# Kernel tuning notes

Measured on AMD Instinct MI355X. Metric: run time of the kernel, lower is better.

## Reference

```python
import jax, jax.numpy as jnp
import numpy as np

T, B = 128, 64
EMB, HID, NTOK = 400, 1152, 33278
# layer dims: (in, out) per layer, matching AWD_LSTM construction
LAYER_DIMS = [(EMB, HID), (HID, HID), (HID, EMB)]


def _uniform(key, shape, bound):
    return jax.random.uniform(key, shape, jnp.float32, -bound, bound)


def setup_inputs() -> dict:
    key = jax.random.key(0)
    ks = jax.random.split(key, 32)
    inp = {
        "x": jax.random.normal(ks[0], (T, B, EMB), jnp.float32),
        "h0_0": jnp.zeros((B, HID), jnp.float32),
        "h0_1": jnp.zeros((B, HID), jnp.float32),
        "h0_2": jnp.zeros((B, EMB), jnp.float32),
        "c0_0": jnp.zeros((B, HID), jnp.float32),
        "c0_1": jnp.zeros((B, HID), jnp.float32),
        "c0_2": jnp.zeros((B, EMB), jnp.float32),
    }
    ki = 1
    for li, (din, dout) in enumerate(LAYER_DIMS):
        bound = 1.0 / np.sqrt(dout)
        inp[f"W_ih{li}"] = _uniform(ks[ki + 0], (4 * dout, din), bound)
        inp[f"W_hh{li}"] = _uniform(ks[ki + 1], (4 * dout, dout), bound)
        inp[f"b_ih{li}"] = _uniform(ks[ki + 2], (4 * dout,), bound)
        inp[f"b_hh{li}"] = _uniform(ks[ki + 3], (4 * dout,), bound)
        ki += 4
    bd = 1.0 / np.sqrt(EMB)
    inp["W_dec"] = _uniform(ks[ki], (NTOK, EMB), bd)
    inp["b_dec"] = _uniform(ks[ki + 1], (NTOK,), bd)
    return inp


def _lstm_cell(x, h, c, W_ih, W_hh, b_ih, b_hh):
    # PyTorch gate order: i, f, g, o
    gates = x @ W_ih.T + b_ih + h @ W_hh.T + b_hh
    i, f, g, o = jnp.split(gates, 4, axis=-1)
    c_new = jax.nn.sigmoid(f) * c + jax.nn.sigmoid(i) * jnp.tanh(g)
    h_new = jax.nn.sigmoid(o) * jnp.tanh(c_new)
    return h_new, c_new


def reference(x, h0_0, h0_1, h0_2, c0_0, c0_1, c0_2,
              W_ih0, W_hh0, b_ih0, b_hh0,
              W_ih1, W_hh1, b_ih1, b_hh1,
              W_ih2, W_hh2, b_ih2, b_hh2,
              W_dec, b_dec):
    params = [(W_ih0, W_hh0, b_ih0, b_hh0),
              (W_ih1, W_hh1, b_ih1, b_hh1),
              (W_ih2, W_hh2, b_ih2, b_hh2)]

    def step(carry, xt):
        hs, cs = carry
        inp = xt
        new_h, new_c = [], []
        for li in range(3):
            h, c = _lstm_cell(inp, hs[li], cs[li], *params[li])
            new_h.append(h)
            new_c.append(c)
            inp = h
        return (tuple(new_h), tuple(new_c)), new_h[-1]

    carry0 = ((h0_0, h0_1, h0_2), (c0_0, c0_1, c0_2))
    (hs, cs), out = jax.lax.scan(step, carry0, x)  # out: (T, B, EMB)
    decoded = out.reshape(T * B, EMB) @ W_dec.T + b_dec
    return decoded.reshape(T, B, NTOK)
```

## Files before the change

kernel.cpp:

```cpp
#include <hip/hip_runtime.h>
#include <math.h>

typedef unsigned short u16;
typedef __attribute__((ext_vector_type(8))) short short8;
typedef __attribute__((ext_vector_type(4))) float f32x4;

__device__ __forceinline__ u16 f32_to_bf16(float x) {
    union { float f; unsigned int u; } v; v.f = x;
    unsigned int u = v.u;
    return (u16)((u + 0x7FFFu + ((u >> 16) & 1u)) >> 16);
}
__device__ __forceinline__ float bf16_to_f32(u16 h) {
    union { unsigned int u; float f; } v; v.u = ((unsigned int)h) << 16; return v.f;
}

__global__ void split_pad_kernel(const float* __restrict__ src,
                                 u16* __restrict__ hi, u16* __restrict__ lo,
                                 int N, int K, int Npad, int Kpad, int perm)
{
    int idx = blockIdx.x * 256 + threadIdx.x;
    if (idx >= Npad * Kpad) return;
    int n = idx / Kpad, k = idx - n * Kpad;
    float x = 0.f;
    if (n < N && k < K) {
        int srow = n;
        if (perm) { int dout = N >> 2; srow = (n & 3) * dout + (n >> 2); }
        x = src[(size_t)srow * K + k];
    }
    u16 h = f32_to_bf16(x);
    hi[idx] = h;
    lo[idx] = f32_to_bf16(x - bf16_to_f32(h));
}

__global__ void bias_perm_kernel(const float* __restrict__ bi,
                                 const float* __restrict__ bh,
                                 float* __restrict__ out, int N4)
{
    int c = blockIdx.x * 256 + threadIdx.x;
    if (c >= N4) return;
    int dout = N4 >> 2;
    int s = (c & 3) * dout + (c >> 2);
    out[c] = bi[s] + bh[s];
}

__global__ __launch_bounds__(256) void gemm3m(
    const float* __restrict__ Af32,
    const u16* __restrict__ Ahi, const u16* __restrict__ Alo,
    const u16* __restrict__ Whi, const u16* __restrict__ Wlo,
    const float* __restrict__ bias,
    float* __restrict__ C,
    int Nreal, int Kreal, int Kp, int lda, int ldc, int amode)
{
    __shared__ __align__(16) u16 As[2][128][32];
    __shared__ __align__(16) u16 Ws[2][128][32];

    const int tid  = threadIdx.x;
    const int lane = tid & 63, wave = tid >> 6;
    const int m0 = blockIdx.y * 128, n0 = blockIdx.x * 128;
    const int wm = (wave >> 1) * 64, wn = (wave & 1) * 64;

    f32x4 acc[4][4];
#pragma unroll
    for (int i = 0; i < 4; ++i)
#pragma unroll
        for (int j = 0; j < 4; ++j)
#pragma unroll
            for (int r = 0; r < 4; ++r) acc[i][j][r] = 0.f;

    const int srow = tid >> 2;
    const int sq   = tid & 3;
    const int dq   = (sq ^ ((srow >> 2) & 3)) * 8;
    const int fr   = lane & 15;
    const int fq   = lane >> 4;
    const int rcol = (fq ^ ((fr >> 2) & 3)) * 8;

    for (int k0 = 0; k0 < Kp; k0 += 32) {
#pragma unroll
        for (int half = 0; half < 2; ++half) {
            int row = half * 64 + srow;
            int kc  = k0 + sq * 8;
            if (amode == 0) {
                union { u16 s[8]; short8 v; } uh, ul;
                if (kc + 8 <= Kreal) {
                    const float* p = &Af32[(size_t)(m0 + row) * lda + kc];
#pragma unroll
                    for (int j = 0; j < 8; ++j) {
                        float xv = p[j];
                        u16 hh = f32_to_bf16(xv);
                        uh.s[j] = hh;
                        ul.s[j] = f32_to_bf16(xv - bf16_to_f32(hh));
                    }
                } else {
#pragma unroll
                    for (int j = 0; j < 8; ++j) { uh.s[j] = 0; ul.s[j] = 0; }
                }
                *(short8*)&As[0][row][dq] = uh.v;
                *(short8*)&As[1][row][dq] = ul.v;
            } else {
                size_t ao = (size_t)(m0 + row) * lda + kc;
                *(short8*)&As[0][row][dq] = *(const short8*)(Ahi + ao);
                *(short8*)&As[1][row][dq] = *(const short8*)(Alo + ao);
            }
            size_t wo = (size_t)(n0 + row) * Kp + kc;
            *(short8*)&Ws[0][row][dq] = *(const short8*)(Whi + wo);
            *(short8*)&Ws[1][row][dq] = *(const short8*)(Wlo + wo);
        }
        __syncthreads();

        short8 ah[4], al[4], wh[4], wl[4];
#pragma unroll
        for (int f = 0; f < 4; ++f) {
            int arow = wm + f * 16 + fr;
            ah[f] = *(const short8*)&As[0][arow][rcol];
            al[f] = *(const short8*)&As[1][arow][rcol];
            int wrow = wn + f * 16 + fr;
            wh[f] = *(const short8*)&Ws[0][wrow][rcol];
            wl[f] = *(const short8*)&Ws[1][wrow][rcol];
        }
#pragma unroll
        for (int i = 0; i < 4; ++i)
#pragma unroll
            for (int j = 0; j < 4; ++j) {
                acc[i][j] = __builtin_amdgcn_mfma_f32_16x16x32_bf16(ah[i], wh[j], acc[i][j], 0, 0, 0);
                acc[i][j] = __builtin_amdgcn_mfma_f32_16x16x32_bf16(ah[i], wl[j], acc[i][j], 0, 0, 0);
                acc[i][j] = __builtin_amdgcn_mfma_f32_16x16x32_bf16(al[i], wh[j], acc[i][j], 0, 0, 0);
            }
        __syncthreads();
    }

#pragma unroll
    for (int j = 0; j < 4; ++j) {
        int n = n0 + wn + j * 16 + fr;
        if (n >= Nreal) continue;
        float bv = bias ? bias[n] : 0.f;
#pragma unroll
        for (int i = 0; i < 4; ++i) {
            int mrow = m0 + wm + i * 16 + fq * 4;
#pragma unroll
            for (int r = 0; r < 4; ++r)
                C[(size_t)(mrow + r) * ldc + n] = acc[i][j][r] + bv;
        }
    }
}

#define PF(S, KT_) do {                                                        \
    int q_ = (((KT_) * 4 + fq) ^ sxor) * 8;                                    \
    a0h_##S = *(const short8*)&Wlds[rA * Kp + q_];                             \
    a0l_##S = *(const short8*)&Wlds[(32 + rA) * Kp + q_];                      \
    a1h_##S = *(const short8*)&Wlds[rB * Kp + q_];                             \
    a1l_##S = *(const short8*)&Wlds[(32 + rB) * Kp + q_];                      \
    hh_##S = *(const short8*)(hrow_hi + (KT_) * 32 + fq * 8);                  \
    hl_##S = *(const short8*)(hrow_lo + (KT_) * 32 + fq * 8);                  \
} while (0)

#define CM(S) do {                                                             \
    accA = __builtin_amdgcn_mfma_f32_16x16x32_bf16(a0h_##S, hh_##S, accA, 0, 0, 0); \
    accB = __builtin_amdgcn_mfma_f32_16x16x32_bf16(a1h_##S, hh_##S, accB, 0, 0, 0); \
    accA = __builtin_amdgcn_mfma_f32_16x16x32_bf16(a0h_##S, hl_##S, accA, 0, 0, 0); \
    accB = __builtin_amdgcn_mfma_f32_16x16x32_bf16(a1h_##S, hl_##S, accB, 0, 0, 0); \
    accA = __builtin_amdgcn_mfma_f32_16x16x32_bf16(a0l_##S, hh_##S, accA, 0, 0, 0); \
    accB = __builtin_amdgcn_mfma_f32_16x16x32_bf16(a1l_##S, hh_##S, accB, 0, 0, 0); \
} while (0)

__global__ __launch_bounds__(256, 1) void persistent_lstm(
    const u16* __restrict__ Whi, const u16* __restrict__ Wlo,
    const u16* __restrict__ h0hi, const u16* __restrict__ h0lo,
    u16* __restrict__ seqHi, u16* __restrict__ seqLo,
    const float* __restrict__ pre,
    const float* __restrict__ c_in, float* __restrict__ c_out,
    int* __restrict__ gcnt,
    int* __restrict__ rootc,
    int* __restrict__ go,
    int t0, int N4, int Kp, int dout, int G)
{
    extern __shared__ __align__(16) u16 Wlds[];
    const int tid  = threadIdx.x;
    const int lane = tid & 63, wave = tid >> 6;
    const int fr = lane & 15, fq = lane >> 4;
    const int c0blk = blockIdx.x * 32;
    const int CH = Kp >> 3;
    const int b = wave * 16 + fr;
    const int grp = blockIdx.x & 7;
    const int gsz = (G - grp + 7) >> 3;

    for (int idx = tid; idx < 64 * CH; idx += 256) {
        int buf = idx / (32 * CH);
        int rem = idx - buf * 32 * CH;
        int r = rem / CH, q = rem - r * CH;
        const u16* src = buf ? Wlo : Whi;
        short8 v = *(const short8*)(src + (size_t)(c0blk + r) * Kp + q * 8);
        *(short8*)&Wlds[(buf * 32 + r) * Kp + (q ^ (r & 7)) * 8] = v;
    }

    const int cA = c0blk + fq * 4;
    const int cB = cA + 16;
    const int jA = cA >> 2, jB = cB >> 2;
    float cregA = c_in[(size_t)b * dout + jA];
    float cregB = c_in[(size_t)b * dout + jB];

    const int rA = fr, rB = 16 + fr;
    const int sxor = fr & 7;
    const int KT = Kp >> 5;
    __syncthreads();

    for (int ts = 0; ts < 64; ++ts) {
        const int t = t0 + ts;
        const u16* hbase_hi = (t == 0) ? h0hi : seqHi + (size_t)(t - 1) * 64 * Kp;
        const u16* hbase_lo = (t == 0) ? h0lo : seqLo + (size_t)(t - 1) * 64 * Kp;
        const u16* hrow_hi = hbase_hi + (size_t)b * Kp;
        const u16* hrow_lo = hbase_lo + (size_t)b * Kp;

        const float* prow = pre + (size_t)(ts * 64 + b) * N4;
        f32x4 preA = *(const f32x4*)(prow + cA);
        f32x4 preB = *(const f32x4*)(prow + cB);

        f32x4 accA = {0.f, 0.f, 0.f, 0.f};
        f32x4 accB = {0.f, 0.f, 0.f, 0.f};
        short8 a0h_0, a0l_0, a1h_0, a1l_0, hh_0, hl_0;
        short8 a0h_1, a0l_1, a1h_1, a1l_1, hh_1, hl_1;
        short8 a0h_2, a0l_2, a1h_2, a1l_2, hh_2, hl_2;
        short8 a0h_3, a0l_3, a1h_3, a1l_3, hh_3, hl_3;
        short8 a0h_4, a0l_4, a1h_4, a1l_4, hh_4, hl_4;
        short8 a0h_5, a0l_5, a1h_5, a1l_5, hh_5, hl_5;

        PF(0, 0); PF(1, 1); PF(2, 2); PF(3, 3); PF(4, 4); PF(5, 5);
        for (int kt = 0; kt < KT - 6; kt += 6) {
            CM(0); PF(0, kt + 6);
            CM(1); PF(1, kt + 7);
            CM(2); PF(2, kt + 8);
            CM(3); PF(3, kt + 9);
            CM(4); PF(4, kt + 10);
            CM(5); PF(5, kt + 11);
        }
        CM(0); CM(1); CM(2); CM(3); CM(4); CM(5);

#pragma unroll
        for (int ct = 0; ct < 2; ++ct) {
            f32x4 a = ct ? accB : accA;
            f32x4 p = ct ? preB : preA;
            int j  = ct ? jB : jA;
            float gi = a[0] + p[0];
            float gf = a[1] + p[1];
            float gg = a[2] + p[2];
            float go_ = a[3] + p[3];
            float si = 1.f / (1.f + expf(-gi));
            float sf = 1.f / (1.f + expf(-gf));
            float so = 1.f / (1.f + expf(-go_));
            float tg = tanhf(gg);
            float cn = sf * (ct ? cregB : cregA) + si * tg;
            float hv = so * tanhf(cn);
            if (ct) cregB = cn; else cregA = cn;
            u16 hb = f32_to_bf16(hv);
            size_t so_ = (size_t)(t * 64 + b) * Kp + j;
            seqHi[so_] = hb;
            seqLo[so_] = f32_to_bf16(hv - bf16_to_f32(hb));
        }

        if (ts != 63) {
            __syncthreads();
            if (tid == 0) {
                __builtin_amdgcn_fence(__ATOMIC_RELEASE, "agent");
                int old = __hip_atomic_fetch_add(&gcnt[(ts * 8 + grp) * 32], 1,
                                                 __ATOMIC_RELAXED, __HIP_MEMORY_SCOPE_AGENT);
                if (old == gsz - 1) {
                    int r = __hip_atomic_fetch_add(&rootc[ts * 32], 1,
                                                   __ATOMIC_RELAXED, __HIP_MEMORY_SCOPE_AGENT);
                    if (r == 7)
                        __hip_atomic_store(&go[ts], 1,
                                           __ATOMIC_RELAXED, __HIP_MEMORY_SCOPE_AGENT);
                }
                while (__hip_atomic_load(&go[ts], __ATOMIC_RELAXED,
                                         __HIP_MEMORY_SCOPE_AGENT) == 0)
                    __builtin_amdgcn_s_sleep(2);
                __builtin_amdgcn_fence(__ATOMIC_ACQUIRE, "agent");
            }
            __syncthreads();
        }
    }

    c_out[(size_t)b * dout + jA] = cregA;
    c_out[(size_t)b * dout + jB] = cregB;
}

extern "C" void kernel_launch(void* const* d_in, const int* in_sizes, int n_in,
                              void* d_out, int out_size, void* d_ws, size_t ws_size,
                              hipStream_t stream)
{
    const int T = 128, B = 64, EMB = 400, HID = 1152, NTOK = 33278;
    const int TB = T * B;

    const float* x     = (const float*)d_in[0];
    const float* h0[3] = {(const float*)d_in[1], (const float*)d_in[2], (const float*)d_in[3]};
    const float* c0[3] = {(const float*)d_in[4], (const float*)d_in[5], (const float*)d_in[6]};
    const float* W_ih[3] = {(const float*)d_in[7],  (const float*)d_in[11], (const float*)d_in[15]};
    const float* W_hh[3] = {(const float*)d_in[8],  (const float*)d_in[12], (const float*)d_in[16]};
    const float* b_ih[3] = {(const float*)d_in[9],  (const float*)d_in[13], (const float*)d_in[17]};
    const float* b_hh[3] = {(const float*)d_in[10], (const float*)d_in[14], (const float*)d_in[18]};
    const float* W_dec = (const float*)d_in[19];
    const float* b_dec = (const float*)d_in[20];

    const int din[3]    = {EMB, HID, HID};
    const int Kpre[3]   = {416, 1152, 1152};
    const int dh[3]     = {HID, HID, EMB};
    const int KpH[3]    = {1152, 1152, 576};
    const int N4[3]     = {4608, 4608, 1600};
    const int N4p128[3] = {4608, 4608, 1664};
    const int Gp[3]     = {144, 144, 50};

    char* wsp = (char*)d_ws;
    size_t off = 0;
    auto alloc = [&](size_t bytes) -> char* {
        char* p = wsp + off; off = (off + bytes + 255) & ~(size_t)255; return p;
    };

    float* pre   = (float*)alloc((size_t)4096 * 4608 * 4);
    u16* seqHi   = (u16*)alloc((size_t)TB * 1152 * 2);
    u16* seqLo   = (u16*)alloc((size_t)TB * 1152 * 2);
    u16* WihHi   = (u16*)alloc((size_t)4608 * 1152 * 2);
    u16* WihLo   = (u16*)alloc((size_t)4608 * 1152 * 2);
    u16* WhhHi   = (u16*)alloc((size_t)4608 * 1152 * 2);
    u16* WhhLo   = (u16*)alloc((size_t)4608 * 1152 * 2);
    u16* h0Hi    = (u16*)alloc((size_t)B * 1152 * 2);
    u16* h0Lo    = (u16*)alloc((size_t)B * 1152 * 2);
    float* bsum  = (float*)alloc(4608 * 4);
    float* cstb  = (float*)alloc((size_t)B * HID * 4);
    const size_t gcntN = (size_t)6 * 64 * 8 * 32;
    const size_t rootN = (size_t)6 * 64 * 32;
    const size_t goN   = (size_t)6 * 64;
    int* syncbuf = (int*)alloc((gcntN + rootN + goN) * 4);
    int* gcnt  = syncbuf;
    int* rootc = syncbuf + gcntN;
    int* go    = syncbuf + gcntN + rootN;
    u16* WdecHi  = (u16*)pre;
    u16* WdecLo  = (u16*)pre + (size_t)33280 * 416;

    hipMemsetAsync(syncbuf, 0, (gcntN + rootN + goN) * 4, stream);
    hipFuncSetAttribute(reinterpret_cast<const void*>(persistent_lstm),
                        hipFuncAttributeMaxDynamicSharedMemorySize, 160 * 1024);

    auto run_split = [&](const float* src, u16* hi, u16* lo,
                         int N, int K, int Npad, int Kpad, int perm) {
        int total = Npad * Kpad;
        split_pad_kernel<<<(total + 255) / 256, 256, 0, stream>>>(
            src, hi, lo, N, K, Npad, Kpad, perm);
    };

    for (int l = 0; l < 3; ++l) {
        run_split(W_hh[l], WhhHi, WhhLo, N4[l], dh[l], N4[l], KpH[l], 1);
        run_split(h0[l], h0Hi, h0Lo, B, dh[l], B, KpH[l], 0);
        run_split(W_ih[l], WihHi, WihLo, N4[l], din[l], N4p128[l], Kpre[l], 1);
        bias_perm_kernel<<<(N4[l] + 255) / 256, 256, 0, stream>>>(
            b_ih[l], b_hh[l], bsum, N4[l]);

        const int ldaA = (l == 0) ? EMB : KpH[l - 1];
        const size_t ldsB = (size_t)128 * KpH[l];

        for (int halfT = 0; halfT < 2; ++halfT) {
            const int li = l * 2 + halfT;
            const float* Af32 = (l == 0) ? (x + (size_t)halfT * 4096 * EMB) : nullptr;
            const u16* Ah = (l == 0) ? nullptr : (seqHi + (size_t)halfT * 4096 * ldaA);
            const u16* Al = (l == 0) ? nullptr : (seqLo + (size_t)halfT * 4096 * ldaA);
            gemm3m<<<dim3(N4p128[l] / 128, 32), 256, 0, stream>>>(
                Af32, Ah, Al, WihHi, WihLo, bsum, pre,
                N4[l], din[l], Kpre[l], ldaA, N4[l], (l == 0) ? 0 : 1);

            const float* cin = (halfT == 0) ? c0[l] : cstb;
            persistent_lstm<<<dim3(Gp[l]), 256, ldsB, stream>>>(
                WhhHi, WhhLo, h0Hi, h0Lo, seqHi, seqLo, pre,
                cin, cstb,
                gcnt + (size_t)li * 64 * 8 * 32,
                rootc + (size_t)li * 64 * 32,
                go + (size_t)li * 64,
                halfT * 64, N4[l], KpH[l], dh[l], Gp[l]);
        }
    }

    run_split(W_dec, WdecHi, WdecLo, NTOK, EMB, 33280, 416, 0);
    gemm3m<<<dim3(260, 64), 256, 0, stream>>>(
        nullptr, seqHi, seqLo, WdecHi, WdecLo, b_dec, (float*)d_out,
        NTOK, EMB, 416, 576, NTOK, 1);
}
```

Before: 6.748 ms.

## Stage GEMM epilogue through LDS, swizzle tile order, prefetch pre, flatten grid barrier

The GEMM epilogue now stages accumulators through shared memory so each thread writes contiguous 16-float row chunks with vector stores, replacing scattered scalar stores. Blocks are launched on a 1D grid and remapped so groups of N-tiles sweep all M-tiles, which is meant to improve L2 reuse of weight tiles. In the persistent LSTM kernel, the next step's pre-activation loads are issued before the grid barrier to hide their latency. The hierarchical counter/root/go barrier is replaced by a flat spin in which thread 0 of every block polls all 8 group counters. The flat barrier drops the explicit acquire fence and adds polling traffic from every block, which could hurt correctness or contention.

```diff
diff --git a/kernel.cpp b/kernel.cpp
--- a/kernel.cpp
+++ b/kernel.cpp
@@ -4,6 +4,7 @@
 typedef unsigned short u16;
 typedef __attribute__((ext_vector_type(8))) short short8;
 typedef __attribute__((ext_vector_type(4))) float f32x4;
+typedef __attribute__((ext_vector_type(2))) float f32x2;
 
 __device__ __forceinline__ u16 f32_to_bf16(float x) {
     union { float f; unsigned int u; } v; v.f = x;
@@ -49,14 +50,24 @@
     const u16* __restrict__ Whi, const u16* __restrict__ Wlo,
     const float* __restrict__ bias,
     float* __restrict__ C,
-    int Nreal, int Kreal, int Kp, int lda, int ldc, int amode)
+    int Nreal, int Kreal, int Kp, int lda, int ldc, int amode,
+    int MT, int NSUB)
 {
-    __shared__ __align__(16) u16 As[2][128][32];
-    __shared__ __align__(16) u16 Ws[2][128][32];
+    extern __shared__ __align__(16) char smem[];
+    u16 (*As)[128][32] = (u16 (*)[128][32])smem;
+    u16 (*Ws)[128][32] = (u16 (*)[128][32])(smem + 16384);
+    float (*Cs)[129]   = (float (*)[129])smem;
 
     const int tid  = threadIdx.x;
     const int lane = tid & 63, wave = tid >> 6;
-    const int m0 = blockIdx.y * 128, n0 = blockIdx.x * 128;
+
+    const int bid   = blockIdx.x;
+    const int super = bid / (NSUB * MT);
+    const int rem   = bid - super * (NSUB * MT);
+    const int mtile = rem / NSUB;
+    const int ntile = super * NSUB + (rem - mtile * NSUB);
+    const int m0 = mtile * 128, n0 = ntile * 128;
+
     const int wm = (wave >> 1) * 64, wn = (wave & 1) * 64;
 
     f32x4 acc[4][4];
@@ -128,17 +139,49 @@
         __syncthreads();
     }
 
-#pragma unroll
-    for (int j = 0; j < 4; ++j) {
-        int n = n0 + wn + j * 16 + fr;
-        if (n >= Nreal) continue;
-        float bv = bias ? bias[n] : 0.f;
-#pragma unroll
-        for (int i = 0; i < 4; ++i) {
-            int mrow = m0 + wm + i * 16 + fq * 4;
+    const int erow = tid & 31;
+    const int echk = tid >> 5;
+    const int gm_base = m0 + ((erow >> 4) * 64) + (erow & 15);
+    const int gn0 = n0 + echk * 16;
+    const bool vec4ok = ((ldc & 3) == 0);
+
+#pragma unroll
+    for (int i = 0; i < 4; ++i) {
+        __syncthreads();
+#pragma unroll
+        for (int j = 0; j < 4; ++j)
 #pragma unroll
             for (int r = 0; r < 4; ++r)
-                C[(size_t)(mrow + r) * ldc + n] = acc[i][j][r] + bv;
+                Cs[(wave >> 1) * 16 + fq * 4 + r][wn + j * 16 + fr] = acc[i][j][r];
+        __syncthreads();
+
+        const int gm = gm_base + i * 16;
+        float* crow = C + (size_t)gm * ldc;
+        if (gn0 + 16 <= Nreal) {
+#pragma unroll
+            for (int q = 0; q < 4; ++q) {
+                f32x4 v = *(const f32x4*)&Cs[erow][echk * 16 + q * 4];
+                if (bias) {
+                    f32x4 bv = *(const f32x4*)&bias[gn0 + q * 4];
+                    v += bv;
+                }
+                if (vec4ok) {
+                    *(f32x4*)&crow[gn0 + q * 4] = v;
+                } else {
+                    f32x2 lo2 = {v[0], v[1]}, hi2 = {v[2], v[3]};
+                    *(f32x2*)&crow[gn0 + q * 4]     = lo2;
+                    *(f32x2*)&crow[gn0 + q * 4 + 2] = hi2;
+                }
+            }
+        } else {
+#pragma unroll
+            for (int q = 0; q < 4; ++q)
+#pragma unroll
+                for (int p = 0; p < 4; ++p) {
+                    int n = gn0 + q * 4 + p;
+                    if (n < Nreal)
+                        crow[n] = Cs[erow][echk * 16 + q * 4 + p] + (bias ? bias[n] : 0.f);
+                }
         }
     }
 }
@@ -169,8 +212,6 @@
     const float* __restrict__ pre,
     const float* __restrict__ c_in, float* __restrict__ c_out,
     int* __restrict__ gcnt,
-    int* __restrict__ rootc,
-    int* __restrict__ go,
     int t0, int N4, int Kp, int dout, int G)
 {
     extern __shared__ __align__(16) u16 Wlds[];
@@ -181,7 +222,6 @@
     const int CH = Kp >> 3;
     const int b = wave * 16 + fr;
     const int grp = blockIdx.x & 7;
-    const int gsz = (G - grp + 7) >> 3;
 
     for (int idx = tid; idx < 64 * CH; idx += 256) {
         int buf = idx / (32 * CH);
@@ -201,6 +241,9 @@
     const int rA = fr, rB = 16 + fr;
     const int sxor = fr & 7;
     const int KT = Kp >> 5;
+
+    f32x4 preA = *(const f32x4*)(pre + (size_t)b * N4 + cA);
+    f32x4 preB = *(const f32x4*)(pre + (size_t)b * N4 + cB);
     __syncthreads();
 
     for (int ts = 0; ts < 64; ++ts) {
@@ -209,10 +252,6 @@
         const u16* hbase_lo = (t == 0) ? h0lo : seqLo + (size_t)(t - 1) * 64 * Kp;
         const u16* hrow_hi = hbase_hi + (size_t)b * Kp;
         const u16* hrow_lo = hbase_lo + (size_t)b * Kp;
-
-        const float* prow = pre + (size_t)(ts * 64 + b) * N4;
-        f32x4 preA = *(const f32x4*)(prow + cA);
-        f32x4 preB = *(const f32x4*)(prow + cB);
 
         f32x4 accA = {0.f, 0.f, 0.f, 0.f};
         f32x4 accB = {0.f, 0.f, 0.f, 0.f};
@@ -258,23 +297,27 @@
 
         if (ts != 63) {
             __syncthreads();
+            {
+                const float* prow2 = pre + (size_t)((ts + 1) * 64 + b) * N4;
+                preA = *(const f32x4*)(prow2 + cA);
+                preB = *(const f32x4*)(prow2 + cB);
+            }
             if (tid == 0) {
                 __builtin_amdgcn_fence(__ATOMIC_RELEASE, "agent");
-                int old = __hip_atomic_fetch_add(&gcnt[(ts * 8 + grp) * 32], 1,
+                __hip_atomic_fetch_add(&gcnt[(ts * 8 + grp) * 32], 1,
+                                       __ATOMIC_RELAXED, __HIP_MEMORY_SCOPE_AGENT);
+                int sum;
+                do {
+                    sum = 0;
+#pragma unroll
+                    for (int g = 0; g < 8; ++g)
+                        sum += __hip_atomic_load(&gcnt[(ts * 8 + g) * 32],
                                                  __ATOMIC_RELAXED, __HIP_MEMORY_SCOPE_AGENT);
-                if (old == gsz - 1) {
-                    int r = __hip_atomic_fetch_add(&rootc[ts * 32], 1,
-                                                   __ATOMIC_RELAXED, __HIP_MEMORY_SCOPE_AGENT);
-                    if (r == 7)
-                        __hip_atomic_store(&go[ts], 1,
-                                           __ATOMIC_RELAXED, __HIP_MEMORY_SCOPE_AGENT);
-                }
-                while (__hip_atomic_load(&go[ts], __ATOMIC_RELAXED,
-                                         __HIP_MEMORY_SCOPE_AGENT) == 0)
-                    __builtin_amdgcn_s_sleep(2);
-                __builtin_amdgcn_fence(__ATOMIC_ACQUIRE, "agent");
+                    if (sum < G) __builtin_amdgcn_s_sleep(1);
+                } while (sum < G);
             }
             __syncthreads();
+            __builtin_amdgcn_sched_barrier(0);
         }
     }
 
@@ -305,6 +348,7 @@
     const int KpH[3]    = {1152, 1152, 576};
     const int N4[3]     = {4608, 4608, 1600};
     const int N4p128[3] = {4608, 4608, 1664};
+    const int NSUBpre[3] = {6, 6, 13};
     const int Gp[3]     = {144, 144, 50};
 
     char* wsp = (char*)d_ws;
@@ -325,18 +369,15 @@
     float* bsum  = (float*)alloc(4608 * 4);
     float* cstb  = (float*)alloc((size_t)B * HID * 4);
     const size_t gcntN = (size_t)6 * 64 * 8 * 32;
-    const size_t rootN = (size_t)6 * 64 * 32;
-    const size_t goN   = (size_t)6 * 64;
-    int* syncbuf = (int*)alloc((gcntN + rootN + goN) * 4);
-    int* gcnt  = syncbuf;
-    int* rootc = syncbuf + gcntN;
-    int* go    = syncbuf + gcntN + rootN;
+    int* gcnt = (int*)alloc(gcntN * 4);
     u16* WdecHi  = (u16*)pre;
     u16* WdecLo  = (u16*)pre + (size_t)33280 * 416;
 
-    hipMemsetAsync(syncbuf, 0, (gcntN + rootN + goN) * 4, stream);
+    hipMemsetAsync(gcnt, 0, gcntN * 4, stream);
     hipFuncSetAttribute(reinterpret_cast<const void*>(persistent_lstm),
                         hipFuncAttributeMaxDynamicSharedMemorySize, 160 * 1024);
+    hipFuncSetAttribute(reinterpret_cast<const void*>(gemm3m),
+                        hipFuncAttributeMaxDynamicSharedMemorySize, 64 * 1024);
 
     auto run_split = [&](const float* src, u16* hi, u16* lo,
                          int N, int K, int Npad, int Kpad, int perm) {
@@ -353,6 +394,7 @@
             b_ih[l], b_hh[l], bsum, N4[l]);
 
         const int ldaA = (l == 0) ? EMB : KpH[l - 1];
+        const int NT = N4p128[l] / 128, MT = 32;
         const size_t ldsB = (size_t)128 * KpH[l];
 
         for (int halfT = 0; halfT < 2; ++halfT) {
@@ -360,23 +402,23 @@
             const float* Af32 = (l == 0) ? (x + (size_t)halfT * 4096 * EMB) : nullptr;
             const u16* Ah = (l == 0) ? nullptr : (seqHi + (size_t)halfT * 4096 * ldaA);
             const u16* Al = (l == 0) ? nullptr : (seqLo + (size_t)halfT * 4096 * ldaA);
-            gemm3m<<<dim3(N4p128[l] / 128, 32), 256, 0, stream>>>(
+            gemm3m<<<dim3(NT * MT), 256, 32768, stream>>>(
                 Af32, Ah, Al, WihHi, WihLo, bsum, pre,
-                N4[l], din[l], Kpre[l], ldaA, N4[l], (l == 0) ? 0 : 1);
+                N4[l], din[l], Kpre[l], ldaA, N4[l], (l == 0) ? 0 : 1,
+                MT, NSUBpre[l]);
 
             const float* cin = (halfT == 0) ? c0[l] : cstb;
             persistent_lstm<<<dim3(Gp[l]), 256, ldsB, stream>>>(
                 WhhHi, WhhLo, h0Hi, h0Lo, seqHi, seqLo, pre,
                 cin, cstb,
                 gcnt + (size_t)li * 64 * 8 * 32,
-                rootc + (size_t)li * 64 * 32,
-                go + (size_t)li * 64,
                 halfT * 64, N4[l], KpH[l], dh[l], Gp[l]);
         }
     }
 
     run_split(W_dec, WdecHi, WdecLo, NTOK, EMB, 33280, 416, 0);
-    gemm3m<<<dim3(260, 64), 256, 0, stream>>>(
+    gemm3m<<<dim3(260 * 64), 256, 32768, stream>>>(
         nullptr, seqHi, seqLo, WdecHi, WdecLo, b_dec, (float*)d_out,
-        NTOK, EMB, 416, 576, NTOK, 1);
-}
+        NTOK, EMB, 416, 576, NTOK, 1,
+        64, 5);
+}
```

New measurement: 6.536 ms. 1.03x faster.
